# Kernel tuning notes

Hardware: AMD Instinct MI355X
Metric: run time of the kernel (lower is better)

Reference implementation:

```python
import jax, jax.numpy as jnp
import numpy as np

PAD = 4  # matches init kwarg


def setup_inputs() -> dict:
    key = jax.random.key(0)
    k1, k2 = jax.random.split(key)
    n, c, h, w = 512, 9, 84, 84
    x = jax.random.normal(k1, (n, c, h, w), dtype=jnp.float32)
    # per-sample integer shift in [0, 2*PAD], last axis = (sx, sy) like grid_sample's (x, y)
    shift = jax.random.randint(k2, (n, 2), 0, 2 * PAD + 1, dtype=jnp.int32)
    return {"x": x, "shift": shift}


def reference(x, shift):
    # Equivalent to: replicate-pad by PAD, then grid_sample(nearest, align_corners=False)
    # with grid = base + integer_shift*2/(h+2*PAD). The grid is constructed so every
    # sample lands exactly on padded-pixel center (i+sy, j+sx), i.e. a pure shifted crop.
    n, c, h, w = x.shape
    p = PAD
    xp = jnp.pad(x, ((0, 0), (0, 0), (p, p), (p, p)), mode='edge')  # replicate pad

    def crop(img, s):
        # img: [c, h+2p, w+2p]; s = (sx, sy)
        return jax.lax.dynamic_slice(img, (0, s[1], s[0]), (c, h, w))

    return jax.vmap(crop)(xp, shift)
```

## Files before the change

### kernel.cpp

```cpp
#include <hip/hip_runtime.h>


#define PADN 4
#define NB   512
#define CB   9
#define HB   84
#define WB   84
#define W4   (WB / 4)

struct __attribute__((packed, aligned(4))) f4u { float a, b, c, d; };

__global__ __launch_bounds__(256) void random_shifts_kernel(
    const float* __restrict__ x,
    const int*   __restrict__ shift,
    float*       __restrict__ out,
    int total )
{
    const int stride = gridDim.x * blockDim.x;
    for (int t = blockIdx.x * blockDim.x + threadIdx.x; t < total; t += stride) {
        const int j4 = t % W4;
        const int r  = t / W4;
        const int i  = r % HB;
        const int nc = r / HB;
        const int n  = nc / CB;

        const int sx = shift[2 * n];
        const int sy = shift[2 * n + 1];

        int si = i + sy - PADN;
        si = si < 0 ? 0 : (si > HB - 1 ? HB - 1 : si);

        const float* srow = x + ((size_t)nc * HB + si) * WB;

        const int j  = j4 * 4;
        const int cs = j + sx - PADN;

        float4 v;
        if (cs >= 0 && cs + 3 <= WB - 1) {
            const f4u u = *reinterpret_cast<const f4u*>(srow + cs);
            v = make_float4(u.a, u.b, u.c, u.d);
        } else {
            const int c0 = min(max(cs,     0), WB - 1);
            const int c1 = min(max(cs + 1, 0), WB - 1);
            const int c2 = min(max(cs + 2, 0), WB - 1);
            const int c3 = min(max(cs + 3, 0), WB - 1);
            v = make_float4(srow[c0], srow[c1], srow[c2], srow[c3]);
        }

        *reinterpret_cast<float4*>(out + (size_t)t * 4) = v;
    }
}

extern "C" void kernel_launch(void* const* d_in, const int* in_sizes, int n_in,
                              void* d_out, int out_size, void* d_ws, size_t ws_size,
                              hipStream_t stream) {
    const float* x     = (const float*)d_in[0];
    const int*   shift = (const int*)d_in[1];
    float*       out   = (float*)d_out;

    const int total = NB * CB * HB * W4;
    const int threads = 256;
    const int blocks  = 2048;
    random_shifts_kernel<<<blocks, threads, 0, stream>>>(x, shift, out, total);
}
```

Before: 227.3 us.

## Map one block per image channel plane with unrolled float4 copies

```diff
diff --git a/kernel.cpp b/kernel.cpp
--- a/kernel.cpp
+++ b/kernel.cpp
@@ -6,48 +6,59 @@
 #define CB   9
 #define HB   84
 #define WB   84
-#define W4   (WB / 4)
+#define W4   21
+#define IMG_F4 (HB * W4)
 
 struct __attribute__((packed, aligned(4))) f4u { float a, b, c, d; };
+
+__device__ __forceinline__ float4 load_shifted(const float* __restrict__ srow, int cs) {
+    if (cs >= 0 && cs <= WB - 4) {
+        const f4u u = *reinterpret_cast<const f4u*>(srow + cs);
+        return make_float4(u.a, u.b, u.c, u.d);
+    }
+    const int c0 = min(max(cs,     0), WB - 1);
+    const int c1 = min(max(cs + 1, 0), WB - 1);
+    const int c2 = min(max(cs + 2, 0), WB - 1);
+    const int c3 = min(max(cs + 3, 0), WB - 1);
+    return make_float4(srow[c0], srow[c1], srow[c2], srow[c3]);
+}
 
 __global__ __launch_bounds__(256) void random_shifts_kernel(
     const float* __restrict__ x,
     const int*   __restrict__ shift,
-    float*       __restrict__ out,
-    int total )
+    float*       __restrict__ out)
 {
-    const int stride = gridDim.x * blockDim.x;
-    for (int t = blockIdx.x * blockDim.x + threadIdx.x; t < total; t += stride) {
-        const int j4 = t % W4;
-        const int r  = t / W4;
-        const int i  = r % HB;
-        const int nc = r / HB;
-        const int n  = nc / CB;
+    const int nc = blockIdx.x;
+    const int n  = nc / CB;
+    const int dx = shift[2 * n]     - PADN;
+    const int dy = shift[2 * n + 1] - PADN;
 
-        const int sx = shift[2 * n];
-        const int sy = shift[2 * n + 1];
+    const float* __restrict__ img = x   + (size_t)nc * (HB * WB);
+    float*       __restrict__ dst = out + (size_t)nc * (HB * WB);
+    const int tid = threadIdx.x;
 
-        int si = i + sy - PADN;
-        si = si < 0 ? 0 : (si > HB - 1 ? HB - 1 : si);
-
-        const float* srow = x + ((size_t)nc * HB + si) * WB;
-
-        const int j  = j4 * 4;
-        const int cs = j + sx - PADN;
-
-        float4 v;
-        if (cs >= 0 && cs + 3 <= WB - 1) {
-            const f4u u = *reinterpret_cast<const f4u*>(srow + cs);
-            v = make_float4(u.a, u.b, u.c, u.d);
-        } else {
-            const int c0 = min(max(cs,     0), WB - 1);
-            const int c1 = min(max(cs + 1, 0), WB - 1);
-            const int c2 = min(max(cs + 2, 0), WB - 1);
-            const int c3 = min(max(cs + 3, 0), WB - 1);
-            v = make_float4(srow[c0], srow[c1], srow[c2], srow[c3]);
+#pragma unroll
+    for (int k = 0; k < 6; ++k) {
+        const int fid = tid + (k << 8);
+        const int i   = fid / W4;
+        const int j4  = fid - i * W4;
+        int si = i + dy;
+        si = min(max(si, 0), HB - 1);
+        const float* srow = img + si * WB;
+        const float4 v = load_shifted(srow, (j4 << 2) + dx);
+        *reinterpret_cast<float4*>(dst + ((size_t)fid << 2)) = v;
+    }
+    {
+        const int fid = tid + (6 << 8);
+        if (fid < IMG_F4) {
+            const int i  = fid / W4;
+            const int j4 = fid - i * W4;
+            int si = i + dy;
+            si = min(max(si, 0), HB - 1);
+            const float* srow = img + si * WB;
+            const float4 v = load_shifted(srow, (j4 << 2) + dx);
+            *reinterpret_cast<float4*>(dst + ((size_t)fid << 2)) = v;
         }
-
-        *reinterpret_cast<float4*>(out + (size_t)t * 4) = v;
     }
 }
 
@@ -58,8 +69,5 @@
     const int*   shift = (const int*)d_in[1];
     float*       out   = (float*)d_out;
 
-    const int total = NB * CB * HB * W4;
-    const int threads = 256;
-    const int blocks  = 2048;
-    random_shifts_kernel<<<blocks, threads, 0, stream>>>(x, shift, out, total);
+    random_shifts_kernel<<<NB * CB, 256, 0, stream>>>(x, shift, out);
 }
```

Result: no change. 231.2 us (+1.7%).

## Map one block per image-channel plane and hoist shift and column math

Applied to the files above, without the earlier changes.

```diff
diff --git a/kernel.cpp b/kernel.cpp
--- a/kernel.cpp
+++ b/kernel.cpp
@@ -1,53 +1,53 @@
 #include <hip/hip_runtime.h>
 
 
-#define PADN 4
-#define NB   512
-#define CB   9
-#define HB   84
-#define WB   84
-#define W4   (WB / 4)
+#define CBn  9
+#define HBn  84
+#define WBn  84
+#define IMG  (HBn * WBn)
 
 struct __attribute__((packed, aligned(4))) f4u { float a, b, c, d; };
 
 __global__ __launch_bounds__(256) void random_shifts_kernel(
     const float* __restrict__ x,
     const int*   __restrict__ shift,
-    float*       __restrict__ out,
-    int total )
+    float*       __restrict__ out)
 {
-    const int stride = gridDim.x * blockDim.x;
-    for (int t = blockIdx.x * blockDim.x + threadIdx.x; t < total; t += stride) {
-        const int j4 = t % W4;
-        const int r  = t / W4;
-        const int i  = r % HB;
-        const int nc = r / HB;
-        const int n  = nc / CB;
+    const int nc = blockIdx.x;
+    const int n  = nc / CBn;
+    const int dx = shift[2 * n]     - 4;
+    const int dy = shift[2 * n + 1] - 4;
 
-        const int sx = shift[2 * n];
-        const int sy = shift[2 * n + 1];
+    const int tid = threadIdx.x;
+    if (tid >= 252) return;
 
-        int si = i + sy - PADN;
-        si = si < 0 ? 0 : (si > HB - 1 ? HB - 1 : si);
+    const int r0 = tid / 21;
+    const int j4 = tid - r0 * 21;
+    const int cs = (j4 << 2) + dx;
 
-        const float* srow = x + ((size_t)nc * HB + si) * WB;
+    const float* __restrict__ img = x   + (size_t)nc * IMG;
+    float*       __restrict__ dst = out + (size_t)nc * IMG + (j4 << 2);
 
-        const int j  = j4 * 4;
-        const int cs = j + sx - PADN;
+    const bool interior = (cs >= 0) & (cs <= WBn - 4);
+    const int c0 = min(max(cs,     0), WBn - 1);
+    const int c1 = min(max(cs + 1, 0), WBn - 1);
+    const int c2 = min(max(cs + 2, 0), WBn - 1);
+    const int c3 = min(max(cs + 3, 0), WBn - 1);
 
+#pragma unroll
+    for (int k = 0; k < 7; ++k) {
+        const int i  = k * 12 + r0;
+        int si = i + dy;
+        si = min(max(si, 0), HBn - 1);
+        const float* srow = img + si * WBn;
         float4 v;
-        if (cs >= 0 && cs + 3 <= WB - 1) {
+        if (interior) {
             const f4u u = *reinterpret_cast<const f4u*>(srow + cs);
             v = make_float4(u.a, u.b, u.c, u.d);
         } else {
-            const int c0 = min(max(cs,     0), WB - 1);
-            const int c1 = min(max(cs + 1, 0), WB - 1);
-            const int c2 = min(max(cs + 2, 0), WB - 1);
-            const int c3 = min(max(cs + 3, 0), WB - 1);
             v = make_float4(srow[c0], srow[c1], srow[c2], srow[c3]);
         }
-
-        *reinterpret_cast<float4*>(out + (size_t)t * 4) = v;
+        *reinterpret_cast<float4*>(dst + i * WBn) = v;
     }
 }
 
@@ -58,8 +58,5 @@
     const int*   shift = (const int*)d_in[1];
     float*       out   = (float*)d_out;
 
-    const int total = NB * CB * HB * W4;
-    const int threads = 256;
-    const int blocks  = 2048;
-    random_shifts_kernel<<<blocks, threads, 0, stream>>>(x, shift, out, total);
+    random_shifts_kernel<<<512 * CBn, 256, 0, stream>>>(x, shift, out);
 }
```

New measurement: 231.3 us. About the same (+1.8%).
